# Kernel tuning notes

Hardware: AMD Instinct MI355X
Metric: run time of the kernel (lower is better)

## Reference

```python
import jax, jax.numpy as jnp
import numpy as np

C, H, W = 16, 128, 128   # in_features, dim0, dim1
FD, OUT, POOL = 3, 64, 2  # filter_dim, out_features, pooling
B = 32


def setup_inputs() -> dict:
    key = jax.random.key(0)
    k1, k2, k3 = jax.random.split(key, 3)
    x = jax.random.normal(k1, (B, C, H, W), dtype=jnp.float32)
    # linear_layer: weight (in*fd^2, out) scaled by 1/sqrt(in*fd^2), bias (out,)
    weight = jax.random.normal(k2, (C * FD * FD, OUT), dtype=jnp.float32) / jnp.sqrt(
        jnp.float32(C * FD * FD))
    bias = jax.random.normal(k3, (OUT,), dtype=jnp.float32)
    return {"x": x, "weight": weight, "bias": bias}


def reference(x, weight, bias):
    # The one-hot isometry tensordot + reshape is exactly im2col with patch
    # vector ordering c*FD^2 + n*FD + m, so the whole convolution() equals a
    # VALID conv with kernel[o, c, n, m] = weight[c*FD^2 + n*FD + m, o].
    kernel = weight.reshape(C, FD, FD, OUT).transpose(3, 0, 1, 2)  # OIHW
    y = jax.lax.conv_general_dilated(
        x, kernel, window_strides=(1, 1), padding='VALID',
        dimension_numbers=('NCHW', 'OIHW', 'NCHW'))  # (B, OUT, n_conv, m_conv)
    y = jax.nn.relu(y + bias[None, :, None, None])
    b, o, hc, wc = y.shape  # hc = H-FD+1 = 126
    # block max-pool POOLxPOOL (crop to multiple of POOL, as in the original)
    hp, wp = hc // POOL, wc // POOL
    y = y[:, :, :hp * POOL, :wp * POOL].reshape(b, o, hp, POOL, wp, POOL)
    y = jnp.max(y, axis=(3, 5))  # (B, OUT, hp, wp)
    return y.reshape(b, o, -1)  # (B, OUT, hp*wp)
```

## Files before the change

### kernel.cpp

```cpp
#include <hip/hip_runtime.h>


typedef _Float16 f16x8 __attribute__((ext_vector_type(8)));
typedef float f32x16 __attribute__((ext_vector_type(16)));

#define MFMA16(A, B, C) __builtin_amdgcn_mfma_f32_32x32x16_f16(A, B, C, 0, 0, 0)
#define XH_BYTES 16777216

#define GLOAD_LDS16(g, l)                                                    \
  __builtin_amdgcn_global_load_lds(                                          \
      (const __attribute__((address_space(1))) void*)(g),                    \
      (__attribute__((address_space(3))) void*)(l), 16, 0, 0)

__global__ void convert_xw(const float* __restrict__ x,
                           const float* __restrict__ weight,
                           char* __restrict__ ws) {
  const int n = blockIdx.x;
  if (n < 4096) {
    const int g = n * 256 + threadIdx.x;
    const int hf = g & 1, col = (g >> 1) & 127, row = (g >> 8) & 127, b = g >> 15;
    _Float16 h[8];
#pragma unroll
    for (int j = 0; j < 8; ++j)
      h[j] = (_Float16)x[((b * 16 + hf * 8 + j) * 128 + row) * 128 + col];
    *(f16x8*)(ws + g * 16) = *(f16x8*)h;
  } else {
    const int tau = (n - 4096) * 256 + threadIdx.x;
    if (tau >= 1152) return;
    const int t = tau >> 7, r = tau & 127, o = r >> 1, hf = r & 1;
    _Float16 h[8];
#pragma unroll
    for (int j = 0; j < 8; ++j)
      h[j] = (_Float16)weight[((hf * 8 + j) * 9 + t) * 64 + o];
    const int off = (t * 2 + (o >> 5)) * 1024 + (hf * 32 + (o & 31)) * 16;
    *(f16x8*)(ws + XH_BYTES + off) = *(f16x8*)h;
  }
}

__global__ __launch_bounds__(256, 4)
void convpool_main(const char* __restrict__ ws, const float* __restrict__ bias,
                   float* __restrict__ out) {
  __shared__ __align__(16) char lds[24640];
  const int tid = threadIdx.x;
  const int bx = blockIdx.x;
  const int oh = bx >> 5;
  const int s = bx & 31;
  const int b = blockIdx.y;
  const int nsteps = (s < 31) ? 2 : 1;
  const int rb = 4 * s;
  const int lane = tid & 63;
  const int ph = tid >> 6;
  const int half = lane >> 5;
  const int c31 = lane & 31;

  const char* xrow = ws + (size_t)(b * 128 + rb) * 4096 + tid * 16;
#pragma unroll
  for (int r = 0; r < 6; ++r)
    if (rb + r < 128)
      GLOAD_LDS16(xrow + r * 4096, lds + r * 4096 + tid * 16);

  const char* wsW = ws + XH_BYTES;
  f16x8 W[9];
#pragma unroll
  for (int t = 0; t < 9; ++t)
    W[t] = *(const f16x8*)(wsW + (t * 2 + oh) * 1024 + lane * 16);

  __syncthreads();

  const int xoff = (ph * 32 + c31) * 32 + half * 16;
  const int pw = ph * 16 + (c31 >> 1);
  const bool doit = ((c31 & 1) == 0) && (pw < 63);

  for (int i = 0; i < nsteps; ++i) {
    f32x16 a0, a1;
#pragma unroll
    for (int q = 0; q < 16; ++q) { a0[q] = 0.f; a1[q] = 0.f; }
    __builtin_amdgcn_s_setprio(1);
#pragma unroll
    for (int t = 0; t < 9; ++t) {
      const int n = t / 3, m = t - 3 * n;
      const int ad = (2 * i + n) * 4096 + xoff + m * 32;
      f16x8 X0 = *(const f16x8*)(lds + ad);
      f16x8 X1 = *(const f16x8*)(lds + ad + 4096);
      a0 = MFMA16(W[t], X0, a0);
      a1 = MFMA16(W[t], X1, a1);
    }
    __builtin_amdgcn_s_setprio(0);

    const int p = 2 * s + i;
    const int obase = ((b * 64) * 63 + p) * 63 + pw;
#pragma unroll
    for (int q = 0; q < 16; ++q) {
      const int o0 = oh * 32 + (q & 3) + 8 * (q >> 2);
      float v = fmaxf(a0[q], a1[q]);
      v = fmaxf(v, __shfl_xor(v, 1, 64));
      const float bv = half ? bias[o0 + 4] : bias[o0];
      v = fmaxf(v + bv, 0.0f);
      if (doit) out[obase + (o0 + 4 * half) * 3969] = v;
    }
  }
}

extern "C" void kernel_launch(void* const* d_in, const int* in_sizes, int n_in,
                              void* d_out, int out_size, void* d_ws, size_t ws_size,
                              hipStream_t stream) {
  const float* x = (const float*)d_in[0];
  const float* wgt = (const float*)d_in[1];
  const float* bias = (const float*)d_in[2];
  float* out = (float*)d_out;
  char* ws = (char*)d_ws;
  convert_xw<<<dim3(4101), 256, 0, stream>>>(x, wgt, ws);
  convpool_main<<<dim3(64, 32), 256, 0, stream>>>(ws, bias, out);
}
```

Before: 39.02 us.

## Load conv input directly from global into registers, drop LDS staging

The main kernel no longer stages six input rows in shared memory through global_load_lds with a barrier. Each thread now reads its 4x3 input fragments straight from global memory into registers for every pooled row. Blocks now cover four pooled rows instead of two, which halves the grid and gives each block more weight reuse. The cost is redundant global and L2 traffic, since neighbouring pooled rows overlap by one input row, and the load latency is no longer hidden behind a shared staging phase.

```diff
diff --git a/kernel.cpp b/kernel.cpp
--- a/kernel.cpp
+++ b/kernel.cpp
@@ -6,11 +6,6 @@
 
 #define MFMA16(A, B, C) __builtin_amdgcn_mfma_f32_32x32x16_f16(A, B, C, 0, 0, 0)
 #define XH_BYTES 16777216
-
-#define GLOAD_LDS16(g, l)                                                    \
-  __builtin_amdgcn_global_load_lds(                                          \
-      (const __attribute__((address_space(1))) void*)(g),                    \
-      (__attribute__((address_space(3))) void*)(l), 16, 0, 0)
 
 __global__ void convert_xw(const float* __restrict__ x,
                            const float* __restrict__ weight,
@@ -40,24 +35,15 @@
 __global__ __launch_bounds__(256, 4)
 void convpool_main(const char* __restrict__ ws, const float* __restrict__ bias,
                    float* __restrict__ out) {
-  __shared__ __align__(16) char lds[24640];
-  const int tid = threadIdx.x;
   const int bx = blockIdx.x;
-  const int oh = bx >> 5;
-  const int s = bx & 31;
+  const int sg = bx >> 1;
+  const int oh = bx & 1;
   const int b = blockIdx.y;
-  const int nsteps = (s < 31) ? 2 : 1;
-  const int rb = 4 * s;
-  const int lane = tid & 63;
-  const int ph = tid >> 6;
+  const int nsteps = (sg < 15) ? 4 : 3;
+  const int lane = threadIdx.x & 63;
+  const int ph = threadIdx.x >> 6;
   const int half = lane >> 5;
   const int c31 = lane & 31;
-
-  const char* xrow = ws + (size_t)(b * 128 + rb) * 4096 + tid * 16;
-#pragma unroll
-  for (int r = 0; r < 6; ++r)
-    if (rb + r < 128)
-      GLOAD_LDS16(xrow + r * 4096, lds + r * 4096 + tid * 16);
 
   const char* wsW = ws + XH_BYTES;
   f16x8 W[9];
@@ -65,13 +51,23 @@
   for (int t = 0; t < 9; ++t)
     W[t] = *(const f16x8*)(wsW + (t * 2 + oh) * 1024 + lane * 16);
 
-  __syncthreads();
+  const char* xbb = ws + (size_t)b * 524288;
+  const int lofs = (ph * 32 + c31) * 32 + half * 16;
 
-  const int xoff = (ph * 32 + c31) * 32 + half * 16;
   const int pw = ph * 16 + (c31 >> 1);
   const bool doit = ((c31 & 1) == 0) && (pw < 63);
 
   for (int i = 0; i < nsteps; ++i) {
+    const int p = 4 * sg + i;
+    const char* rbase = xbb + (size_t)(2 * p) * 4096 + lofs;
+
+    f16x8 X[4][3];
+#pragma unroll
+    for (int r = 0; r < 4; ++r)
+#pragma unroll
+      for (int m = 0; m < 3; ++m)
+        X[r][m] = *(const f16x8*)(rbase + r * 4096 + m * 32);
+
     f32x16 a0, a1;
 #pragma unroll
     for (int q = 0; q < 16; ++q) { a0[q] = 0.f; a1[q] = 0.f; }
@@ -79,15 +75,11 @@
 #pragma unroll
     for (int t = 0; t < 9; ++t) {
       const int n = t / 3, m = t - 3 * n;
-      const int ad = (2 * i + n) * 4096 + xoff + m * 32;
-      f16x8 X0 = *(const f16x8*)(lds + ad);
-      f16x8 X1 = *(const f16x8*)(lds + ad + 4096);
-      a0 = MFMA16(W[t], X0, a0);
-      a1 = MFMA16(W[t], X1, a1);
+      a0 = MFMA16(W[t], X[n][m], a0);
+      a1 = MFMA16(W[t], X[n + 1][m], a1);
     }
     __builtin_amdgcn_s_setprio(0);
 
-    const int p = 2 * s + i;
     const int obase = ((b * 64) * 63 + p) * 63 + pw;
 #pragma unroll
     for (int q = 0; q < 16; ++q) {
@@ -110,5 +102,5 @@
   float* out = (float*)d_out;
   char* ws = (char*)d_ws;
   convert_xw<<<dim3(4101), 256, 0, stream>>>(x, wgt, ws);
-  convpool_main<<<dim3(64, 32), 256, 0, stream>>>(ws, bias, out);
+  convpool_main<<<dim3(32, 32), 256, 0, stream>>>(ws, bias, out);
 }
```

Result: slower. 41.39 us (+6.1%).
